# Kernel optimization log

Measured on AMD Instinct MI355X. Metric: run time of the kernel, lower is better.

## Reference

```python
import jax, jax.numpy as jnp
import numpy as np

# ---- static configuration (matches init_kwargs) ----
B = 32
H = 56
W = 56
C = 192
HEADS = 6
WS = 7            # window size
SHIFT = 3         # shift size (WS // 2)
MLP_HIDDEN = 768  # 4 * C
CPB = 256         # clip(56*56//16, 256, 1024)
N = WS * WS       # tokens per window
NW = (H // WS) * (W // WS)  # windows per image
EPS = 1e-5

# ---- static tables (Swin V2 continuous relative position bias) ----
# log-spaced relative coords table: [(2*WS-1)^2, 2]
_r = np.arange(-(WS - 1), WS, dtype=np.float32)
_tab = np.stack(np.meshgrid(_r, _r, indexing='ij'), axis=-1)  # [2WS-1, 2WS-1, 2]
_tab = _tab / (WS - 1) * 8.0  # pretrained_window_size=0 -> use window_size-1
_tab = np.sign(_tab) * np.log2(np.abs(_tab) + 1.0) / np.log2(8.0)
REL_TABLE = jnp.asarray(_tab.reshape(-1, 2))

# relative position index: [N, N] into the (2WS-1)^2 table
_coords = np.stack(np.meshgrid(np.arange(WS), np.arange(WS), indexing='ij'))
_cf = _coords.reshape(2, -1)
_rel = (_cf[:, :, None] - _cf[:, None, :]).transpose(1, 2, 0).astype(np.int64)
_rel[..., 0] += WS - 1
_rel[..., 1] += WS - 1
_rel[..., 0] *= 2 * WS - 1
REL_INDEX = jnp.asarray(_rel.sum(-1))

# shifted-window attention mask: [NW, N, N] with 0 / -100
_img = np.zeros((H, W), dtype=np.float32)
_sl = [slice(0, -WS), slice(-WS, -SHIFT), slice(-SHIFT, None)]
_cnt = 0
for _hs in _sl:
    for _ws in _sl:
        _img[_hs, _ws] = _cnt
        _cnt += 1
_mw = _img.reshape(H // WS, WS, W // WS, WS).transpose(0, 2, 1, 3).reshape(-1, N)
_am = _mw[:, None, :] - _mw[:, :, None]
ATTN_MASK = jnp.asarray(np.where(_am != 0, -100.0, 0.0).astype(np.float32))


def _layer_norm(x, g, b):
    mu = jnp.mean(x, axis=-1, keepdims=True)
    var = jnp.mean(jnp.square(x - mu), axis=-1, keepdims=True)
    return (x - mu) * jax.lax.rsqrt(var + EPS) * g + b


def setup_inputs() -> dict:
    key = jax.random.key(0)
    ks = jax.random.split(key, 10)
    def n(k, shape, s=0.02):
        return jax.random.normal(k, shape, jnp.float32) * s
    return {
        'x': jax.random.normal(ks[0], (B, H * W, C), jnp.float32),
        'qkv_w': n(ks[1], (3 * C, C)),
        'q_bias': jnp.zeros((C,), jnp.float32),
        'v_bias': jnp.zeros((C,), jnp.float32),
        'logit_scale': jnp.full((HEADS, 1, 1), jnp.log(10.0), jnp.float32),
        'cpb_w1': n(ks[2], (CPB, 2)),
        'cpb_b1': jnp.zeros((CPB,), jnp.float32),
        'cpb_w2': n(ks[3], (HEADS, CPB)),
        'proj_w': n(ks[4], (C, C)),
        'proj_b': jnp.zeros((C,), jnp.float32),
        'norm1_g': jnp.ones((C,), jnp.float32),
        'norm1_b': jnp.zeros((C,), jnp.float32),
        'norm2_g': jnp.ones((C,), jnp.float32),
        'norm2_b': jnp.zeros((C,), jnp.float32),
        'fc1_w': n(ks[5], (MLP_HIDDEN, C)),
        'fc1_b': jnp.zeros((MLP_HIDDEN,), jnp.float32),
        'fc2_w': n(ks[6], (C, MLP_HIDDEN)),
        'fc2_b': jnp.zeros((C,), jnp.float32),
    }


def reference(x, qkv_w, q_bias, v_bias, logit_scale, cpb_w1, cpb_b1, cpb_w2,
              proj_w, proj_b, norm1_g, norm1_b, norm2_g, norm2_b,
              fc1_w, fc1_b, fc2_w, fc2_b):
    b = x.shape[0]
    hd = C // HEADS
    shortcut = x

    # cyclic shift + window partition -> [b*NW, N, C]
    xi = jnp.roll(x.reshape(b, H, W, C), (-SHIFT, -SHIFT), axis=(1, 2))
    xw = xi.reshape(b, H // WS, WS, W // WS, WS, C)
    xw = xw.transpose(0, 1, 3, 2, 4, 5).reshape(-1, N, C)

    # qkv projection (k has no bias, per Swin V2)
    qkv_bias = jnp.concatenate([q_bias, jnp.zeros_like(q_bias), v_bias])
    qkv = (xw @ qkv_w.T + qkv_bias).reshape(-1, N, 3, HEADS, hd)
    qkv = qkv.transpose(2, 0, 3, 1, 4)  # [3, bw, heads, N, hd]
    q, k, v = qkv[0], qkv[1], qkv[2]

    # cosine attention with learned logit scale
    q = q / jnp.maximum(jnp.linalg.norm(q, axis=-1, keepdims=True), 1e-12)
    k = k / jnp.maximum(jnp.linalg.norm(k, axis=-1, keepdims=True), 1e-12)
    scale = jnp.exp(jnp.minimum(logit_scale, jnp.log(100.0)))  # [heads,1,1]
    attn = jnp.einsum('bhnd,bhmd->bhnm', q, k) * scale

    # continuous relative position bias via tiny MLP
    tab = jax.nn.relu(REL_TABLE @ cpb_w1.T + cpb_b1) @ cpb_w2.T  # [(2WS-1)^2, heads]
    rpb = 16.0 * jax.nn.sigmoid(tab[REL_INDEX])                  # [N, N, heads]
    attn = attn + rpb.transpose(2, 0, 1)[None]

    # shifted-window mask + softmax
    attn = attn.reshape(-1, NW, HEADS, N, N) + ATTN_MASK[None, :, None]
    attn = jax.nn.softmax(attn.reshape(-1, HEADS, N, N), axis=-1)

    out = jnp.einsum('bhnm,bhmd->bhnd', attn, v)
    out = out.transpose(0, 2, 1, 3).reshape(-1, N, C) @ proj_w.T + proj_b

    # window reverse + reverse shift
    xr = out.reshape(b, H // WS, W // WS, WS, WS, C)
    xr = xr.transpose(0, 1, 3, 2, 4, 5).reshape(b, H, W, C)
    xr = jnp.roll(xr, (SHIFT, SHIFT), axis=(1, 2)).reshape(b, H * W, C)

    # post-norm residual (Swin V2 style)
    x1 = shortcut + _layer_norm(xr, norm1_g, norm1_b)
    hmid = jax.nn.silu(x1 @ fc1_w.T + fc1_b) @ fc2_w.T + fc2_b
    return x1 + _layer_norm(hmid, norm2_g, norm2_b)
```

## Files before the change

kernel.cpp:

```cpp
#include <hip/hip_runtime.h>


typedef unsigned short ushort_t;
using f32x4  = __attribute__((ext_vector_type(4))) float;
using short8 = __attribute__((ext_vector_type(8))) short;
union LD16 { short8 v; ushort4 h[2]; };

__device__ __forceinline__ ushort_t f2bf(float f) {
  union { float f; unsigned u; } v; v.f = f;
  unsigned r = v.u + 0x7fffu + ((v.u >> 16) & 1u);
  return (ushort_t)(r >> 16);
}
__device__ __forceinline__ float bf2f(ushort_t u) {
  union { unsigned u; float f; } v; v.u = ((unsigned)u) << 16;
  return v.f;
}

__device__ __forceinline__ int img_pos(int m) {
  int win = m / 49, n = m - win * 49;
  int b = win >> 6, wi = win & 63;
  int nd = n / 7, nm = n - nd * 7;
  int hs = (wi >> 3) * 7 + nd;
  int ws = (wi & 7) * 7 + nm;
  int h = hs + 3; if (h >= 56) h -= 56;
  int w = ws + 3; if (w >= 56) w -= 56;
  return b * 3136 + h * 56 + w;
}

__device__ __forceinline__ int region3(int a) { return a < 49 ? 0 : (a < 53 ? 1 : 2); }

__global__ void cvt_kernel(const float* __restrict__ in, ushort_t* __restrict__ out, int n) {
  int i = blockIdx.x * 256 + threadIdx.x;
  if (i < n) out[i] = f2bf(in[i]);
}

__global__ __launch_bounds__(256) void gather_cvt_kernel(
    const float* __restrict__ x, ushort_t* __restrict__ xw) {
  int i8 = blockIdx.x * 256 + threadIdx.x;
  int m = i8 / 24, c8 = (i8 - m * 24) * 8;
  const float* p = x + (size_t)img_pos(m) * 192 + c8;
  float4 a = *(const float4*)p, b = *(const float4*)(p + 4);
  ushort_t* q = xw + (size_t)m * 192 + c8;
  *(ushort4*)q       = make_ushort4(f2bf(a.x), f2bf(a.y), f2bf(a.z), f2bf(a.w));
  *(ushort4*)(q + 4) = make_ushort4(f2bf(b.x), f2bf(b.y), f2bf(b.z), f2bf(b.w));
}

__global__ __launch_bounds__(256) void cpb_kernel(
    const float* __restrict__ w1, const float* __restrict__ b1,
    const float* __restrict__ w2, float* __restrict__ tab_s) {
  int e = blockIdx.x;
  int t = threadIdx.x;
  int i = e / 13, j = e - 13 * (e / 13);
  auto cval = [](int a) -> float {
    float r = (a - 6) * (8.0f / 6.0f);
    float v = log2f(fabsf(r) + 1.f) * (1.f / 3.f);
    return r < 0.f ? -v : v;
  };
  float ci = cval(i), cj = cval(j);
  float h = fmaxf(ci * w1[2 * t] + cj * w1[2 * t + 1] + b1[t], 0.f);
  __shared__ float red[256];
  for (int head = 0; head < 6; ++head) {
    red[t] = h * w2[head * 256 + t];
    __syncthreads();
    for (int st = 128; st > 0; st >>= 1) {
      if (t < st) red[t] += red[t + st];
      __syncthreads();
    }
    if (t == 0) tab_s[head * 169 + e] = 16.f / (1.f + __expf(-red[0]));
    __syncthreads();
  }
}

template<int KTOT, int MODE>
__global__ __launch_bounds__(512, 4) void gemm_n192(
    const ushort_t* __restrict__ Ab, const ushort_t* __restrict__ W,
    const float* __restrict__ b0, const float* __restrict__ b1,
    ushort_t* out, float* outf, int NTOT) {
  __shared__ ushort_t Al[128][40];
  __shared__ ushort_t Bl[192][40];
  int t = threadIdx.x;
  int m0 = blockIdx.x * 128, n0 = blockIdx.y * 192;
  int lane = t & 63, wid = t >> 6;
  int wm = wid >> 1, wn = wid & 1;
  int lr = lane & 15, lg = lane >> 4;

  bool stager = (t < 256);
  int arow = (t & 255) >> 1, akoff = (t & 1) << 4;
  const ushort_t* Arowp = Ab + (size_t)(m0 + arow) * KTOT + akoff;
  int colA = akoff ? 4 : 0;
  int bn = (t & 255) >> 2, cB = t & 3;
  const ushort_t* Browp  = W + (size_t)(n0 + bn) * KTOT + (cB << 3);
  const ushort_t* Browp2 = W + (size_t)(n0 + 64 + bn) * KTOT + (cB << 3);
  const ushort_t* Browp3 = W + (size_t)(n0 + 128 + bn) * KTOT + (cB << 3);
  int colB = ((cB & 1) << 4) | ((cB >> 1) << 2);

  f32x4 acc[2][6];
#pragma unroll
  for (int a = 0; a < 2; ++a)
#pragma unroll
    for (int b = 0; b < 6; ++b) acc[a][b] = (f32x4){0.f, 0.f, 0.f, 0.f};

  LD16 A01, A23, B0, B1, B2;
  auto LOADREGS = [&](int kt) {
    A01.v = *(const short8*)(Arowp + kt);
    A23.v = *(const short8*)(Arowp + kt + 8);
    B0.v  = *(const short8*)(Browp + kt);
    B1.v  = *(const short8*)(Browp2 + kt);
    B2.v  = *(const short8*)(Browp3 + kt);
  };

  const int NT = KTOT / 32;
  if (stager) LOADREGS(0);
  for (int it = 0; it < NT; ++it) {
    if (stager) {
      ushort_t* Ar = &Al[arow][0];
      *(ushort4*)(Ar + colA +  0) = A01.h[0];
      *(ushort4*)(Ar + colA +  8) = A01.h[1];
      *(ushort4*)(Ar + colA + 16) = A23.h[0];
      *(ushort4*)(Ar + colA + 24) = A23.h[1];
      ushort_t* Br0 = &Bl[bn][0];
      *(ushort4*)(Br0 + colB + 0) = B0.h[0];
      *(ushort4*)(Br0 + colB + 8) = B0.h[1];
      ushort_t* Br1 = &Bl[64 + bn][0];
      *(ushort4*)(Br1 + colB + 0) = B1.h[0];
      *(ushort4*)(Br1 + colB + 8) = B1.h[1];
      ushort_t* Br2 = &Bl[128 + bn][0];
      *(ushort4*)(Br2 + colB + 0) = B2.h[0];
      *(ushort4*)(Br2 + colB + 8) = B2.h[1];
    }
    __syncthreads();
    if (stager && it + 1 < NT) LOADREGS((it + 1) * 32);
    short8 af[2], bfv[6];
#pragma unroll
    for (int fm = 0; fm < 2; ++fm)
      af[fm] = *(const short8*)&Al[wm * 32 + fm * 16 + lr][lg * 8];
#pragma unroll
    for (int fn = 0; fn < 6; ++fn)
      bfv[fn] = *(const short8*)&Bl[wn * 96 + fn * 16 + lr][lg * 8];
#pragma unroll
    for (int fm = 0; fm < 2; ++fm)
#pragma unroll
      for (int fn = 0; fn < 6; ++fn)
        acc[fm][fn] = __builtin_amdgcn_mfma_f32_16x16x32_bf16(af[fm], bfv[fn], acc[fm][fn], 0, 0, 0);
    if (it + 1 < NT) __syncthreads();
  }
#pragma unroll
  for (int fm = 0; fm < 2; ++fm) {
#pragma unroll
    for (int fn = 0; fn < 6; ++fn) {
      int col = n0 + wn * 96 + fn * 16 + lr;
      float bias;
      if (MODE == 0) bias = (col < 192) ? b0[col] : ((col < 384) ? 0.f : b1[col - 384]);
      else           bias = b0[col];
#pragma unroll
      for (int r = 0; r < 4; ++r) {
        int row = m0 + wm * 32 + fm * 16 + lg * 4 + r;
        float v = acc[fm][fn][r] + bias;
        if (MODE == 1) v = v / (1.f + __expf(-v));
        if (MODE == 3) outf[(size_t)row * NTOT + col] = v;
        else           out[(size_t)row * NTOT + col] = f2bf(v);
      }
    }
  }
}

template<int MODE>
__global__ __launch_bounds__(256) void ln_resid_kernel(
    const ushort_t* __restrict__ pre, const float* __restrict__ residf,
    const ushort_t* __restrict__ residb, const float* __restrict__ gamma,
    const float* __restrict__ beta, ushort_t* __restrict__ outb,
    float* outio) {
  int m = (blockIdx.x * 256 + threadIdx.x) >> 6;
  int lane = threadIdx.x & 63;
  float v0, v1, v2;
  if (MODE == 0) {
    const ushort_t* p = pre + (size_t)m * 192;
    v0 = bf2f(p[lane]); v1 = bf2f(p[lane + 64]); v2 = bf2f(p[lane + 128]);
  } else {
    const float* p = outio + (size_t)m * 192;
    v0 = p[lane]; v1 = p[lane + 64]; v2 = p[lane + 128];
  }
  float s1 = v0 + v1 + v2;
  float s2 = v0 * v0 + v1 * v1 + v2 * v2;
#pragma unroll
  for (int o = 1; o < 64; o <<= 1) {
    s1 += __shfl_xor(s1, o);
    s2 += __shfl_xor(s2, o);
  }
  float mean = s1 * (1.f / 192.f);
  float var  = s2 * (1.f / 192.f) - mean * mean;
  float rstd = rsqrtf(fmaxf(var, 0.f) + 1e-5f);
  float l0 = (v0 - mean) * rstd * gamma[lane]       + beta[lane];
  float l1 = (v1 - mean) * rstd * gamma[lane + 64]  + beta[lane + 64];
  float l2 = (v2 - mean) * rstd * gamma[lane + 128] + beta[lane + 128];
  if (MODE == 0) {
    size_t og = (size_t)img_pos(m) * 192;
    outb[og + lane]       = f2bf(residf[og + lane]       + l0);
    outb[og + lane + 64]  = f2bf(residf[og + lane + 64]  + l1);
    outb[og + lane + 128] = f2bf(residf[og + lane + 128] + l2);
  } else {
    size_t og = (size_t)m * 192;
    outio[og + lane]       = bf2f(residb[og + lane])       + l0;
    outio[og + lane + 64]  = bf2f(residb[og + lane + 64])  + l1;
    outio[og + lane + 128] = bf2f(residb[og + lane + 128]) + l2;
  }
}

__global__ __launch_bounds__(256) void attn_kernel(
    const ushort_t* __restrict__ qkv, const float* __restrict__ logit_scale,
    const float* __restrict__ tab_s, ushort_t* __restrict__ attn_out) {
  __shared__ ushort_t qs[64][40];
  __shared__ ushort_t ksl[64][40];
  __shared__ ushort_t vsl[32][80];
  __shared__ ushort_t ps[64][80];
  __shared__ float tab_l[169];
  int win = blockIdx.x, head = blockIdx.y;
  int t = threadIdx.x;
  int wi = win & 63;
  int wh0 = (wi >> 3) * 7, ww0 = (wi & 7) * 7;
  size_t base = (size_t)win * 49 * 576 + head * 32;

  for (int u = t; u < 169; u += 256) tab_l[u] = tab_s[head * 169 + u];

  for (int u = t; u < 240; u += 256) {
    int arr = u / 120, v = u - arr * 120;
    int r = 49 + (v >> 3), c4 = (v & 7) << 2;
    ushort_t* p = arr ? &ksl[r][c4] : &qs[r][c4];
    *(ushort4*)p = make_ushort4(0, 0, 0, 0);
  }

  for (int u = t; u < 2048; u += 256) {
    int key = u >> 5, d = u & 31;
    ushort_t val = 0;
    if (key < 49) val = qkv[base + (size_t)key * 576 + 384 + d];
    int kk = key & 31;
    int pc = ((key >> 5) << 5) + 8 * ((kk >> 2) & 3) + 4 * (kk >> 4) + (kk & 3);
    vsl[d][pc] = val;
  }

  float scale = __expf(fminf(logit_scale[head], 4.605170186f));

  if (t < 196) {
    int r = t >> 2, c = t & 3;
    const ushort_t* qp = qkv + base + (size_t)r * 576 + c * 8;
    ushort4 qa = *(const ushort4*)qp,         qb = *(const ushort4*)(qp + 4);
    ushort4 ka = *(const ushort4*)(qp + 192), kb = *(const ushort4*)(qp + 196);
    float qf[8] = {bf2f(qa.x), bf2f(qa.y), bf2f(qa.z), bf2f(qa.w),
                   bf2f(qb.x), bf2f(qb.y), bf2f(qb.z), bf2f(qb.w)};
    float kf[8] = {bf2f(ka.x), bf2f(ka.y), bf2f(ka.z), bf2f(ka.w),
                   bf2f(kb.x), bf2f(kb.y), bf2f(kb.z), bf2f(kb.w)};
    float sq = 0.f, sk = 0.f;
#pragma unroll
    for (int d = 0; d < 8; ++d) { sq += qf[d] * qf[d]; sk += kf[d] * kf[d]; }
    sq += __shfl_xor(sq, 1); sq += __shfl_xor(sq, 2);
    sk += __shfl_xor(sk, 1); sk += __shfl_xor(sk, 2);
    float rq = scale / fmaxf(sqrtf(sq), 1e-12f);
    float rk = 1.f   / fmaxf(sqrtf(sk), 1e-12f);
    int c0 = ((c & 1) << 4) | ((c >> 1) << 2);
    ushort_t* qd = &qs[r][c0];
    *(ushort4*)(qd + 0) = make_ushort4(f2bf(qf[0]*rq), f2bf(qf[1]*rq), f2bf(qf[2]*rq), f2bf(qf[3]*rq));
    *(ushort4*)(qd + 8) = make_ushort4(f2bf(qf[4]*rq), f2bf(qf[5]*rq), f2bf(qf[6]*rq), f2bf(qf[7]*rq));
    ushort_t* kd = &ksl[r][c0];
    *(ushort4*)(kd + 0) = make_ushort4(f2bf(kf[0]*rk), f2bf(kf[1]*rk), f2bf(kf[2]*rk), f2bf(kf[3]*rk));
    *(ushort4*)(kd + 8) = make_ushort4(f2bf(kf[4]*rk), f2bf(kf[5]*rk), f2bf(kf[6]*rk), f2bf(kf[7]*rk));
  }
  __syncthreads();

  int lane = t & 63, w = t >> 6;
  int lr = lane & 15, lg = lane >> 4;

  short8 aq = *(const short8*)&qs[w * 16 + lr][lg * 8];
  f32x4 acc[4];
#pragma unroll
  for (int fn = 0; fn < 4; ++fn) {
    acc[fn] = (f32x4){0.f, 0.f, 0.f, 0.f};
    short8 bk = *(const short8*)&ksl[fn * 16 + lr][lg * 8];
    acc[fn] = __builtin_amdgcn_mfma_f32_16x16x32_bf16(aq, bk, acc[fn], 0, 0, 0);
  }

  float rsum[4];
#pragma unroll
  for (int r = 0; r < 4; ++r) {
    int row = w * 16 + lg * 4 + r;
    int rd = (row * 9363) >> 16, rm = row - 7 * rd;
    int gr = region3(wh0 + rd) * 3 + region3(ww0 + rm);
    bool rv = row < 49;
    float sv[4];
#pragma unroll
    for (int fn = 0; fn < 4; ++fn) {
      int col = fn * 16 + lr;
      int jd = (col * 9363) >> 16, jm = col - 7 * jd;
      int gj = region3(wh0 + jd) * 3 + region3(ww0 + jm);
      bool cv = rv && (col < 49);
      int idx = cv ? (rd - jd + 6) * 13 + (rm - jm + 6) : 0;
      float s = acc[fn][r] + tab_l[idx] + (gr == gj ? 0.f : -100.f);
      sv[fn] = cv ? s : -1e30f;
    }
    float m = fmaxf(fmaxf(sv[0], sv[1]), fmaxf(sv[2], sv[3]));
#pragma unroll
    for (int o = 1; o < 16; o <<= 1) m = fmaxf(m, __shfl_xor(m, o));
    float sum = 0.f;
#pragma unroll
    for (int fn = 0; fn < 4; ++fn) {
      float e = __expf(sv[fn] - m);
      sum += e;
      int pc = ((fn >> 1) << 5) + 8 * (lr >> 2) + ((fn & 1) << 2) + (lr & 3);
      ps[row][pc] = f2bf(e);
    }
#pragma unroll
    for (int o = 1; o < 16; o <<= 1) sum += __shfl_xor(sum, o);
    rsum[r] = 1.f / sum;
  }
  __syncthreads();

  short8 ap0 = *(const short8*)&ps[w * 16 + lr][lg * 8];
  short8 ap1 = *(const short8*)&ps[w * 16 + lr][32 + lg * 8];
  f32x4 o2[2];
#pragma unroll
  for (int f = 0; f < 2; ++f) {
    o2[f] = (f32x4){0.f, 0.f, 0.f, 0.f};
    short8 bv0 = *(const short8*)&vsl[f * 16 + lr][lg * 8];
    short8 bv1 = *(const short8*)&vsl[f * 16 + lr][32 + lg * 8];
    o2[f] = __builtin_amdgcn_mfma_f32_16x16x32_bf16(ap0, bv0, o2[f], 0, 0, 0);
    o2[f] = __builtin_amdgcn_mfma_f32_16x16x32_bf16(ap1, bv1, o2[f], 0, 0, 0);
  }
#pragma unroll
  for (int f = 0; f < 2; ++f) {
#pragma unroll
    for (int r = 0; r < 4; ++r) {
      int row = w * 16 + lg * 4 + r;
      if (row < 49)
        attn_out[((size_t)win * 49 + row) * 192 + head * 32 + f * 16 + lr] =
            f2bf(o2[f][r] * rsum[r]);
    }
  }
}

extern "C" void kernel_launch(void* const* d_in, const int* in_sizes, int n_in,
                              void* d_out, int out_size, void* d_ws, size_t ws_size,
                              hipStream_t stream) {
  (void)in_sizes; (void)n_in; (void)out_size; (void)ws_size;
  const float* x    = (const float*)d_in[0];
  const float* qkvw = (const float*)d_in[1];
  const float* qb   = (const float*)d_in[2];
  const float* vb   = (const float*)d_in[3];
  const float* ls   = (const float*)d_in[4];
  const float* cw1  = (const float*)d_in[5];
  const float* cb1  = (const float*)d_in[6];
  const float* cw2  = (const float*)d_in[7];
  const float* pw   = (const float*)d_in[8];
  const float* pb   = (const float*)d_in[9];
  const float* n1g  = (const float*)d_in[10];
  const float* n1b  = (const float*)d_in[11];
  const float* n2g  = (const float*)d_in[12];
  const float* n2b  = (const float*)d_in[13];
  const float* f1w  = (const float*)d_in[14];
  const float* f1b  = (const float*)d_in[15];
  const float* f2w  = (const float*)d_in[16];
  const float* f2b  = (const float*)d_in[17];
  float* out = (float*)d_out;

  char* ws = (char*)d_ws;
  ushort_t* wq_bf = (ushort_t*)ws;
  ushort_t* wp_bf = wq_bf + 110592;
  ushort_t* w1_bf = wp_bf + 36864;
  ushort_t* w2_bf = w1_bf + 147456;
  float*    tab_s = (float*)(w2_bf + 147456);
  const size_t OFF_BIG = 1 << 20;
  ushort_t* qkv_out = (ushort_t*)(ws + OFF_BIG);
  ushort_t* xw_bf   = (ushort_t*)(ws + OFF_BIG + 115605504);
  ushort_t* attn_o  = (ushort_t*)(ws + OFF_BIG + 115605504);
  ushort_t* x1_bf   = (ushort_t*)(ws + OFF_BIG + 154140672);
  ushort_t* hmid    = (ushort_t*)(ws + OFF_BIG);

  cvt_kernel<<<(110592 + 255) / 256, 256, 0, stream>>>(qkvw, wq_bf, 110592);
  cvt_kernel<<<(36864  + 255) / 256, 256, 0, stream>>>(pw,   wp_bf, 36864);
  cvt_kernel<<<(147456 + 255) / 256, 256, 0, stream>>>(f1w,  w1_bf, 147456);
  cvt_kernel<<<(147456 + 255) / 256, 256, 0, stream>>>(f2w,  w2_bf, 147456);
  cpb_kernel<<<169, 256, 0, stream>>>(cw1, cb1, cw2, tab_s);
  gather_cvt_kernel<<<9408, 256, 0, stream>>>(x, xw_bf);

  gemm_n192<192, 0><<<dim3(784, 3), 512, 0, stream>>>(xw_bf, wq_bf, qb, vb, qkv_out, nullptr, 576);
  attn_kernel<<<dim3(2048, 6), 256, 0, stream>>>(qkv_out, ls, tab_s, attn_o);
  gemm_n192<192, 2><<<dim3(784, 1), 512, 0, stream>>>(attn_o, wp_bf, pb, nullptr, attn_o, nullptr, 192);
  ln_resid_kernel<0><<<25088, 256, 0, stream>>>(attn_o, x, nullptr, n1g, n1b, x1_bf, nullptr);
  gemm_n192<192, 1><<<dim3(784, 4), 512, 0, stream>>>(x1_bf, w1_bf, f1b, nullptr, hmid, nullptr, 768);
  gemm_n192<768, 3><<<dim3(784, 1), 512, 0, stream>>>(hmid, w2_bf, f2b, nullptr, nullptr, out, 192);
  ln_resid_kernel<1><<<25088, 256, 0, stream>>>(nullptr, nullptr, x1_bf, n2g, n2b, nullptr, out);
}
```

Before: 402.7 us.

## Keep the A tile resident in LDS and loop over N chunks in the GEMMs

Adds a GEMM kernel that loads the whole 128x192 A tile into LDS once, then loops over output column chunks of 192, streaming only the B tiles. This replaces the 2D grid that reloaded the same A rows for every N block in the QKV, proj and fc1 GEMMs. The fc2 GEMM becomes its own specialised kernel. The trade-off is more LDS per block, which lowers occupancy, plus fewer, longer blocks with no overlap of the initial A load.

```diff
diff --git a/kernel.cpp b/kernel.cpp
--- a/kernel.cpp
+++ b/kernel.cpp
@@ -71,15 +71,110 @@
   }
 }
 
-template<int KTOT, int MODE>
-__global__ __launch_bounds__(512, 4) void gemm_n192(
+template<int NCHUNK, int MODE>
+__global__ __launch_bounds__(512, 4) void gemm_persistA(
     const ushort_t* __restrict__ Ab, const ushort_t* __restrict__ W,
     const float* __restrict__ b0, const float* __restrict__ b1,
-    ushort_t* out, float* outf, int NTOT) {
+    ushort_t* __restrict__ out, int NTOT) {
+  __shared__ ushort_t Al[128][200];
+  __shared__ ushort_t Bl[192][40];
+  int t = threadIdx.x;
+  int m0 = blockIdx.x * 128;
+  int lane = t & 63, wid = t >> 6;
+  int wm = wid >> 1, wn = wid & 1;
+  int lr = lane & 15, lg = lane >> 4;
+
+#pragma unroll
+  for (int s = 0; s < 6; ++s) {
+    int task = t + (s << 9);
+    int row = task / 24, j = task - row * 24;
+    int blk = (j >> 2) << 5, jj = j & 3;
+    int b4 = ((jj & 1) << 4) | ((jj >> 1) << 2);
+    LD16 v; v.v = *(const short8*)(Ab + (size_t)(m0 + row) * 192 + j * 8);
+    *(ushort4*)&Al[row][blk + b4]     = v.h[0];
+    *(ushort4*)&Al[row][blk + b4 + 8] = v.h[1];
+  }
+
+  bool stager = (t < 256);
+  int bn = (t & 255) >> 2, cB = t & 3;
+  int colB = ((cB & 1) << 4) | ((cB >> 1) << 2);
+
+  for (int c = 0; c < NCHUNK; ++c) {
+    int n0 = c * 192;
+    const ushort_t* Browp  = W + (size_t)(n0 + bn) * 192 + (cB << 3);
+    const ushort_t* Browp2 = W + (size_t)(n0 + 64 + bn) * 192 + (cB << 3);
+    const ushort_t* Browp3 = W + (size_t)(n0 + 128 + bn) * 192 + (cB << 3);
+    LD16 B0, B1, B2;
+    auto LOADB = [&](int kt) {
+      B0.v = *(const short8*)(Browp + kt);
+      B1.v = *(const short8*)(Browp2 + kt);
+      B2.v = *(const short8*)(Browp3 + kt);
+    };
+
+    f32x4 acc[2][6];
+#pragma unroll
+    for (int a = 0; a < 2; ++a)
+#pragma unroll
+      for (int b = 0; b < 6; ++b) acc[a][b] = (f32x4){0.f, 0.f, 0.f, 0.f};
+
+    if (stager) LOADB(0);
+    for (int it = 0; it < 6; ++it) {
+      if (stager) {
+        ushort_t* Br0 = &Bl[bn][0];
+        *(ushort4*)(Br0 + colB + 0) = B0.h[0];
+        *(ushort4*)(Br0 + colB + 8) = B0.h[1];
+        ushort_t* Br1 = &Bl[64 + bn][0];
+        *(ushort4*)(Br1 + colB + 0) = B1.h[0];
+        *(ushort4*)(Br1 + colB + 8) = B1.h[1];
+        ushort_t* Br2 = &Bl[128 + bn][0];
+        *(ushort4*)(Br2 + colB + 0) = B2.h[0];
+        *(ushort4*)(Br2 + colB + 8) = B2.h[1];
+      }
+      __syncthreads();
+      if (stager && it + 1 < 6) LOADB((it + 1) * 32);
+      short8 af[2], bfv[6];
+#pragma unroll
+      for (int fm = 0; fm < 2; ++fm)
+        af[fm] = *(const short8*)&Al[wm * 32 + fm * 16 + lr][it * 32 + lg * 8];
+#pragma unroll
+      for (int fn = 0; fn < 6; ++fn)
+        bfv[fn] = *(const short8*)&Bl[wn * 96 + fn * 16 + lr][lg * 8];
+#pragma unroll
+      for (int fm = 0; fm < 2; ++fm)
+#pragma unroll
+        for (int fn = 0; fn < 6; ++fn)
+          acc[fm][fn] = __builtin_amdgcn_mfma_f32_16x16x32_bf16(af[fm], bfv[fn], acc[fm][fn], 0, 0, 0);
+      __syncthreads();
+    }
+
+#pragma unroll
+    for (int fm = 0; fm < 2; ++fm) {
+#pragma unroll
+      for (int fn = 0; fn < 6; ++fn) {
+        int col = n0 + wn * 96 + fn * 16 + lr;
+        float bias;
+        if (MODE == 0) bias = (col < 192) ? b0[col] : ((col < 384) ? 0.f : b1[col - 384]);
+        else           bias = b0[col];
+#pragma unroll
+        for (int r = 0; r < 4; ++r) {
+          int row = m0 + wm * 32 + fm * 16 + lg * 4 + r;
+          float v = acc[fm][fn][r] + bias;
+          if (MODE == 1) v = v / (1.f + __expf(-v));
+          out[(size_t)row * NTOT + col] = f2bf(v);
+        }
+      }
+    }
+  }
+}
+
+__global__ __launch_bounds__(512, 4) void gemm_fc2(
+    const ushort_t* __restrict__ Ab, const ushort_t* __restrict__ W,
+    const float* __restrict__ b0, float* __restrict__ outf) {
+  const int KTOT = 768, NTOT = 192;
   __shared__ ushort_t Al[128][40];
   __shared__ ushort_t Bl[192][40];
   int t = threadIdx.x;
-  int m0 = blockIdx.x * 128, n0 = blockIdx.y * 192;
+  int m0 = blockIdx.x * 128;
   int lane = t & 63, wid = t >> 6;
   int wm = wid >> 1, wn = wid & 1;
   int lr = lane & 15, lg = lane >> 4;
@@ -89,9 +184,9 @@
   const ushort_t* Arowp = Ab + (size_t)(m0 + arow) * KTOT + akoff;
   int colA = akoff ? 4 : 0;
   int bn = (t & 255) >> 2, cB = t & 3;
-  const ushort_t* Browp  = W + (size_t)(n0 + bn) * KTOT + (cB << 3);
-  const ushort_t* Browp2 = W + (size_t)(n0 + 64 + bn) * KTOT + (cB << 3);
-  const ushort_t* Browp3 = W + (size_t)(n0 + 128 + bn) * KTOT + (cB << 3);
+  const ushort_t* Browp  = W + (size_t)(bn) * KTOT + (cB << 3);
+  const ushort_t* Browp2 = W + (size_t)(64 + bn) * KTOT + (cB << 3);
+  const ushort_t* Browp3 = W + (size_t)(128 + bn) * KTOT + (cB << 3);
   int colB = ((cB & 1) << 4) | ((cB >> 1) << 2);
 
   f32x4 acc[2][6];
@@ -148,17 +243,12 @@
   for (int fm = 0; fm < 2; ++fm) {
 #pragma unroll
     for (int fn = 0; fn < 6; ++fn) {
-      int col = n0 + wn * 96 + fn * 16 + lr;
-      float bias;
-      if (MODE == 0) bias = (col < 192) ? b0[col] : ((col < 384) ? 0.f : b1[col - 384]);
-      else           bias = b0[col];
+      int col = wn * 96 + fn * 16 + lr;
+      float bias = b0[col];
 #pragma unroll
       for (int r = 0; r < 4; ++r) {
         int row = m0 + wm * 32 + fm * 16 + lg * 4 + r;
-        float v = acc[fm][fn][r] + bias;
-        if (MODE == 1) v = v / (1.f + __expf(-v));
-        if (MODE == 3) outf[(size_t)row * NTOT + col] = v;
-        else           out[(size_t)row * NTOT + col] = f2bf(v);
+        outf[(size_t)row * NTOT + col] = acc[fm][fn][r] + bias;
       }
     }
   }
@@ -380,11 +470,11 @@
   cpb_kernel<<<169, 256, 0, stream>>>(cw1, cb1, cw2, tab_s);
   gather_cvt_kernel<<<9408, 256, 0, stream>>>(x, xw_bf);
 
-  gemm_n192<192, 0><<<dim3(784, 3), 512, 0, stream>>>(xw_bf, wq_bf, qb, vb, qkv_out, nullptr, 576);
+  gemm_persistA<3, 0><<<784, 512, 0, stream>>>(xw_bf, wq_bf, qb, vb, qkv_out, 576);
   attn_kernel<<<dim3(2048, 6), 256, 0, stream>>>(qkv_out, ls, tab_s, attn_o);
-  gemm_n192<192, 2><<<dim3(784, 1), 512, 0, stream>>>(attn_o, wp_bf, pb, nullptr, attn_o, nullptr, 192);
+  gemm_persistA<1, 2><<<784, 512, 0, stream>>>(attn_o, wp_bf, pb, nullptr, attn_o, 192);
   ln_resid_kernel<0><<<25088, 256, 0, stream>>>(attn_o, x, nullptr, n1g, n1b, x1_bf, nullptr);
-  gemm_n192<192, 1><<<dim3(784, 4), 512, 0, stream>>>(x1_bf, w1_bf, f1b, nullptr, hmid, nullptr, 768);
-  gemm_n192<768, 3><<<dim3(784, 1), 512, 0, stream>>>(hmid, w2_bf, f2b, nullptr, nullptr, out, 192);
+  gemm_persistA<4, 1><<<784, 512, 0, stream>>>(x1_bf, w1_bf, f1b, nullptr, hmid, 768);
+  gemm_fc2<<<784, 512, 0, stream>>>(hmid, w2_bf, f2b, out);
   ln_resid_kernel<1><<<25088, 256, 0, stream>>>(nullptr, nullptr, x1_bf, n2g, n2b, nullptr, out);
 }
```

New measurement: 400.4 us. No clear change (-0.6%).
